# Performance work log

Hardware: AMD Instinct MI355X
Metric: run time of the kernel (lower is better)

The kernel has to match this reference:

```python
import jax, jax.numpy as jnp
import numpy as np

FEATURE_DIM = 1024
N_HEADS = 16
D_K = 64
D_V = 64
B = 8
S = 1024
LN_EPS = 1e-5
NEG = 1e9


def setup_inputs() -> dict:
    key = jax.random.key(0)
    ks = jax.random.split(key, 7)
    sc = 0.02
    return {
        "input_Q": jax.random.normal(ks[0], (B, S, FEATURE_DIM), jnp.float32),
        "input_K": jax.random.normal(ks[1], (B, S, FEATURE_DIM), jnp.float32),
        "input_V": jax.random.normal(ks[2], (B, S, FEATURE_DIM), jnp.float32),
        "attn_mask": jnp.ones((B, S, S), jnp.float32),
        "W_Q": jax.random.normal(ks[3], (FEATURE_DIM, N_HEADS * D_K), jnp.float32) * sc,
        "W_K": jax.random.normal(ks[4], (FEATURE_DIM, N_HEADS * D_K), jnp.float32) * sc,
        "W_V": jax.random.normal(ks[5], (FEATURE_DIM, N_HEADS * D_V), jnp.float32) * sc,
        "W_O": jax.random.normal(ks[6], (N_HEADS * D_V, FEATURE_DIM), jnp.float32) * sc,
    }


def reference(input_Q, input_K, input_V, attn_mask, W_Q, W_K, W_V, W_O):
    b = input_Q.shape[0]
    # projections -> [b, h, s, d]
    Q = (input_Q @ W_Q).reshape(b, -1, N_HEADS, D_K).transpose(0, 2, 1, 3)
    K = (input_K @ W_K).reshape(b, -1, N_HEADS, D_K).transpose(0, 2, 1, 3)
    V = (input_V @ W_V).reshape(b, -1, N_HEADS, D_V).transpose(0, 2, 1, 3)
    # scores [b, h, sq, sk]
    scores = jnp.einsum("bhqd,bhkd->bhqk", Q, K) / np.sqrt(D_K).astype(np.float32)
    # additive mask: (mask - 1) * 1e9, broadcast over heads
    scores = scores + (attn_mask[:, None, :, :] - 1.0) * NEG
    attn = jax.nn.softmax(scores, axis=-1)
    # dropout is eval-mode identity (deterministic baseline)
    context = jnp.einsum("bhqk,bhkd->bhqd", attn, V)
    context = context.transpose(0, 2, 1, 3).reshape(b, -1, N_HEADS * D_V)
    output = context @ W_O
    x = output + input_Q  # residual
    # fresh nn.LayerNorm(feature_dim): weight=1, bias=0
    mu = jnp.mean(x, axis=-1, keepdims=True)
    var = jnp.var(x, axis=-1, keepdims=True)
    out = (x - mu) * jax.lax.rsqrt(var + LN_EPS)
    return out, attn
```

## Files before the change

### kernel.cpp

```cpp
#include <hip/hip_runtime.h>
#include <hip/hip_bf16.h>
#include <stdint.h>

typedef unsigned short u16;
typedef unsigned int u32;
typedef __attribute__((ext_vector_type(8))) short bf16x8;
typedef __attribute__((ext_vector_type(4))) float f32x4;

#define BATCH 8
#define SEQ   1024
#define FDIM  1024
#define NHEAD 16
#define DHEAD 64

__device__ __forceinline__ float bf2f(u16 u) {
  union { unsigned int i; float f; } v; v.i = ((unsigned int)u) << 16; return v.f;
}
__device__ __forceinline__ u16 f2bf(float f) {
  union { float f; unsigned int i; } v; v.f = f;
  unsigned int x = v.i;
  return (u16)((x + 0x7fffu + ((x >> 16) & 1u)) >> 16);
}

__device__ __forceinline__ uint4 load8(const u16* p) { return *(const uint4*)p; }
__device__ __forceinline__ uint4 load8(const float* p) {
  float4 a = *(const float4*)p;
  float4 b = *(const float4*)(p + 4);
  union { u16 h[8]; uint4 v; } r;
  r.h[0] = f2bf(a.x); r.h[1] = f2bf(a.y); r.h[2] = f2bf(a.z); r.h[3] = f2bf(a.w);
  r.h[4] = f2bf(b.x); r.h[5] = f2bf(b.y); r.h[6] = f2bf(b.z); r.h[7] = f2bf(b.w);
  return r.v;
}

__device__ __forceinline__ void gload16(const u16* g, u16* l) {
  __builtin_amdgcn_global_load_lds(
      (__attribute__((address_space(1))) u32*)(u16*)g,
      (__attribute__((address_space(3))) u32*)l, 16, 0, 0);
}

__global__ __launch_bounds__(256) void cvt_k(
    const float* __restrict__ in, u16* __restrict__ out) {
  const long i = ((long)blockIdx.x * 256 + threadIdx.x) * 8;
  *(uint4*)&out[i] = load8(&in[i]);
}

__global__ __launch_bounds__(256) void transpose_k(
    const float* __restrict__ src, u16* __restrict__ dst, int srcLd, int dstLd) {
  __shared__ u16 t[64][72];
  const int r0 = blockIdx.y * 64, c0 = blockIdx.x * 64;
  const int tid = threadIdx.x;
  for (int p = 0; p < 16; ++p) {
    int idx = p * 256 + tid, r = idx >> 6, c = idx & 63;
    t[r][c] = f2bf(src[(long)(r0 + r) * srcLd + (c0 + c)]);
  }
  __syncthreads();
  for (int p = 0; p < 16; ++p) {
    int idx = p * 256 + tid, r = idx >> 6, c = idx & 63;
    dst[(long)(c0 + r) * dstLd + (r0 + c)] = t[c][r];
  }
}

template<int MODE>
__global__ __launch_bounds__(256) void gemm16(
    const u16* __restrict__ A, const u16* __restrict__ Bt, void* __restrict__ C,
    int K, int lda, int ldb, int ldc) {
  __shared__ __align__(16) u16 As[128 * 32];
  __shared__ __align__(16) u16 Bs[128 * 32];
  const int tid = threadIdx.x;
  const int wave = tid >> 6, lane = tid & 63;
  const int quad = lane >> 4, l16 = lane & 15;
  const int wm = wave >> 1, wn = wave & 1;
  const int bid = blockIdx.y * 8 + blockIdx.x;
  const int cpx = (gridDim.y * 8) >> 3;
  const int swz = (bid & 7) * cpx + (bid >> 3);
  const int m0 = (swz >> 3) * 128, n0 = (swz & 7) * 128;

  f32x4 acc[4][4];
#pragma unroll
  for (int i = 0; i < 4; ++i)
#pragma unroll
    for (int j = 0; j < 4; ++j) acc[i][j] = (f32x4){0.f, 0.f, 0.f, 0.f};

  const int srow = lane >> 2, scol = (lane & 3) * 8;
  const u16* ga = &A[(long)(m0 + wave * 32 + srow) * lda + scol];
  const u16* gb = &Bt[(long)(n0 + wave * 32 + srow) * ldb + scol];
  u16* la0 = &As[(wave * 32) * 32];
  u16* la1 = &As[(wave * 32 + 16) * 32];
  u16* lb0 = &Bs[(wave * 32) * 32];
  u16* lb1 = &Bs[(wave * 32 + 16) * 32];

  for (int k0 = 0; k0 < K; k0 += 32) {
    __syncthreads();
    gload16(ga + k0,            la0);
    gload16(ga + k0 + 16 * lda, la1);
    gload16(gb + k0,            lb0);
    gload16(gb + k0 + 16 * ldb, lb1);
    __syncthreads();
    bf16x8 af[4], bfr[4];
#pragma unroll
    for (int i = 0; i < 4; ++i)
      af[i] = *(const bf16x8*)&As[(wm * 64 + i * 16 + l16) * 32 + quad * 8];
#pragma unroll
    for (int j = 0; j < 4; ++j)
      bfr[j] = *(const bf16x8*)&Bs[(wn * 64 + j * 16 + l16) * 32 + quad * 8];
#pragma unroll
    for (int i = 0; i < 4; ++i)
#pragma unroll
      for (int j = 0; j < 4; ++j)
        acc[i][j] = __builtin_amdgcn_mfma_f32_16x16x32_bf16(af[i], bfr[j], acc[i][j], 0, 0, 0);
  }

#pragma unroll
  for (int i = 0; i < 4; ++i) {
    const int rowb = m0 + wm * 64 + i * 16 + quad * 4;
#pragma unroll
    for (int j = 0; j < 4; ++j) {
      const int col = n0 + wn * 64 + j * 16 + l16;
#pragma unroll
      for (int r = 0; r < 4; ++r) {
        const float v = acc[i][j][r];
        const int row = rowb + r;
        if (MODE == 1) {
          ((float*)C)[(long)row * ldc + col] = v;
        } else if (MODE == 2) {
          int bb = row >> 10, ss = row & 1023, hh = col >> 6, dd = col & 63;
          ((u16*)C)[((long)(bb * NHEAD + hh) * SEQ + ss) * DHEAD + dd] = f2bf(v);
        } else if (MODE == 3) {
          int bb = row >> 10, ss = row & 1023, hh = col >> 6, dd = col & 63;
          ((u16*)C)[((long)(bb * NHEAD + hh) * DHEAD + dd) * SEQ + ss] = f2bf(v);
        } else {
          ((u16*)C)[(long)row * ldc + col] = f2bf(v);
        }
      }
    }
  }
}

__global__ __launch_bounds__(256, 4) void attn_kernel(
    const u16* __restrict__ Qb, const u16* __restrict__ Kb,
    const u16* __restrict__ Vt, const float* __restrict__ Msk,
    float* __restrict__ P, u16* __restrict__ Ctx) {
  __shared__ __align__(16) u16 QVs[64][72];
  __shared__ __align__(16) u16 Ks[64][72];
  __shared__ __align__(16) float Ps[64][68];
  const int tid = threadIdx.x, wave = tid >> 6, lane = tid & 63;
  const int quad = lane >> 4, l16 = lane & 15;
  const int q0 = blockIdx.x * 64, h = blockIdx.y, b = blockIdx.z;
  const long bh = (long)b * NHEAD + h;
  const u16* Qp = Qb + ((long)b * SEQ + q0) * FDIM + h * DHEAD;
  const u16* Kp = Kb + bh * SEQ * DHEAD;
  const u16* Vp = Vt + bh * (long)DHEAD * SEQ;
  const float* Mp = Msk + ((long)b * SEQ + q0) * SEQ;
  float* Pp = P + bh * (long)SEQ * SEQ + (long)q0 * SEQ;
  u16* Cp = Ctx + ((long)b * SEQ + q0) * FDIM + h * DHEAD;

  {
    int r = tid >> 3, c = (tid & 7) * 8;
    *(uint4*)&QVs[r][c]      = *(const uint4*)&Qp[(long)r * FDIM + c];
    *(uint4*)&QVs[r + 32][c] = *(const uint4*)&Qp[(long)(r + 32) * FDIM + c];
  }
  __syncthreads();
  const bf16x8 aq0 = *(const bf16x8*)&QVs[wave * 16 + l16][quad * 8];
  const bf16x8 aq1 = *(const bf16x8*)&QVs[wave * 16 + l16][32 + quad * 8];

  float m[4], l[4], rl[4];
#pragma unroll
  for (int r = 0; r < 4; ++r) { m[r] = -3.0e38f; l[r] = 0.f; }

  for (int st = 0; st < SEQ / 64; ++st) {
    const int sk0 = st * 64;
    __syncthreads();
    {
      int r = tid >> 3, c = (tid & 7) * 8;
      *(uint4*)&Ks[r][c]      = *(const uint4*)&Kp[(sk0 + r) * DHEAD + c];
      *(uint4*)&Ks[r + 32][c] = *(const uint4*)&Kp[(sk0 + r + 32) * DHEAD + c];
    }
    __syncthreads();
    float sv[4][4];
#pragma unroll
    for (int j = 0; j < 4; ++j) {
      bf16x8 bk0 = *(const bf16x8*)&Ks[j * 16 + l16][quad * 8];
      bf16x8 bk1 = *(const bf16x8*)&Ks[j * 16 + l16][32 + quad * 8];
      f32x4 sc = (f32x4){0.f, 0.f, 0.f, 0.f};
      sc = __builtin_amdgcn_mfma_f32_16x16x32_bf16(aq0, bk0, sc, 0, 0, 0);
      sc = __builtin_amdgcn_mfma_f32_16x16x32_bf16(aq1, bk1, sc, 0, 0, 0);
#pragma unroll
      for (int r = 0; r < 4; ++r) {
        int qr = wave * 16 + quad * 4 + r;
        float mk = Mp[(long)qr * SEQ + sk0 + j * 16 + l16];
        sv[j][r] = sc[r] * 0.125f + (mk - 1.0f) * 1.0e9f;
      }
    }
#pragma unroll
    for (int r = 0; r < 4; ++r) {
      float tm = fmaxf(fmaxf(sv[0][r], sv[1][r]), fmaxf(sv[2][r], sv[3][r]));
#pragma unroll
      for (int off = 1; off < 16; off <<= 1) tm = fmaxf(tm, __shfl_xor(tm, off, 64));
      float mn = fmaxf(m[r], tm);
      float ps = __expf(sv[0][r] - mn) + __expf(sv[1][r] - mn) +
                 __expf(sv[2][r] - mn) + __expf(sv[3][r] - mn);
#pragma unroll
      for (int off = 1; off < 16; off <<= 1) ps += __shfl_xor(ps, off, 64);
      l[r] = l[r] * __expf(m[r] - mn) + ps;
      m[r] = mn;
    }
  }
#pragma unroll
  for (int r = 0; r < 4; ++r) rl[r] = 1.0f / l[r];

  f32x4 acc[4];
#pragma unroll
  for (int n = 0; n < 4; ++n) acc[n] = (f32x4){0.f, 0.f, 0.f, 0.f};

  for (int st = 0; st < SEQ / 64; ++st) {
    const int sk0 = st * 64;
    __syncthreads();
    {
      int r = tid >> 3, c = (tid & 7) * 8;
      *(uint4*)&Ks[r][c]       = *(const uint4*)&Kp[(sk0 + r) * DHEAD + c];
      *(uint4*)&Ks[r + 32][c]  = *(const uint4*)&Kp[(sk0 + r + 32) * DHEAD + c];
      *(uint4*)&QVs[r][c]      = *(const uint4*)&Vp[(long)r * SEQ + sk0 + c];
      *(uint4*)&QVs[r + 32][c] = *(const uint4*)&Vp[(long)(r + 32) * SEQ + sk0 + c];
    }
    __syncthreads();
#pragma unroll
    for (int j = 0; j < 4; ++j) {
      bf16x8 bk0 = *(const bf16x8*)&Ks[j * 16 + l16][quad * 8];
      bf16x8 bk1 = *(const bf16x8*)&Ks[j * 16 + l16][32 + quad * 8];
      f32x4 sc = (f32x4){0.f, 0.f, 0.f, 0.f};
      sc = __builtin_amdgcn_mfma_f32_16x16x32_bf16(aq0, bk0, sc, 0, 0, 0);
      sc = __builtin_amdgcn_mfma_f32_16x16x32_bf16(aq1, bk1, sc, 0, 0, 0);
#pragma unroll
      for (int r = 0; r < 4; ++r) {
        int qr = wave * 16 + quad * 4 + r;
        float mk = Mp[(long)qr * SEQ + sk0 + j * 16 + l16];
        float s = sc[r] * 0.125f + (mk - 1.0f) * 1.0e9f;
        Ps[qr][j * 16 + l16] = __expf(s - m[r]) * rl[r];
      }
    }
    __syncthreads();
#pragma unroll
    for (int ks = 0; ks < 2; ++ks) {
      const float* pr = &Ps[wave * 16 + l16][ks * 32 + quad * 8];
      f32x4 plo = *(const f32x4*)pr;
      f32x4 phi = *(const f32x4*)(pr + 4);
      union { u16 h[8]; bf16x8 v; } pa;
      pa.h[0] = f2bf(plo.x); pa.h[1] = f2bf(plo.y);
      pa.h[2] = f2bf(plo.z); pa.h[3] = f2bf(plo.w);
      pa.h[4] = f2bf(phi.x); pa.h[5] = f2bf(phi.y);
      pa.h[6] = f2bf(phi.z); pa.h[7] = f2bf(phi.w);
#pragma unroll
      for (int n = 0; n < 4; ++n) {
        bf16x8 bv = *(const bf16x8*)&QVs[n * 16 + l16][ks * 32 + quad * 8];
        acc[n] = __builtin_amdgcn_mfma_f32_16x16x32_bf16(pa.v, bv, acc[n], 0, 0, 0);
      }
    }
#pragma unroll
    for (int rr = 0; rr < 4; ++rr) {
      const int row = wave * 16 + rr * 4 + quad;
      f32x4 val = *(const f32x4*)&Ps[row][l16 * 4];
      __builtin_nontemporal_store(val, (f32x4*)&Pp[(long)row * SEQ + sk0 + l16 * 4]);
    }
  }

#pragma unroll
  for (int n = 0; n < 4; ++n)
#pragma unroll
    for (int r = 0; r < 4; ++r)
      Cp[(long)(wave * 16 + quad * 4 + r) * FDIM + n * 16 + l16] = f2bf(acc[n][r]);
}

__global__ __launch_bounds__(256) void ln_kernel(
    const float* __restrict__ O, const float* __restrict__ Xq, float* __restrict__ out) {
  const int row = blockIdx.x, tid = threadIdx.x;
  const float4 o = *(const float4*)&O[(long)row * FDIM + tid * 4];
  const float4 q = *(const float4*)&Xq[(long)row * FDIM + tid * 4];
  float x[4] = { o.x + q.x, o.y + q.y, o.z + q.z, o.w + q.w };
  float s  = x[0] + x[1] + x[2] + x[3];
  float s2 = x[0]*x[0] + x[1]*x[1] + x[2]*x[2] + x[3]*x[3];
#pragma unroll
  for (int off = 32; off; off >>= 1) {
    s  += __shfl_xor(s, off, 64);
    s2 += __shfl_xor(s2, off, 64);
  }
  __shared__ float red[8];
  const int wave = tid >> 6, lane = tid & 63;
  if (lane == 0) { red[wave] = s; red[4 + wave] = s2; }
  __syncthreads();
  s  = red[0] + red[1] + red[2] + red[3];
  s2 = red[4] + red[5] + red[6] + red[7];
  const float mu = s * (1.0f / FDIM);
  const float var = s2 * (1.0f / FDIM) - mu * mu;
  const float rs = rsqrtf(var + 1e-5f);
  float4 res;
  res.x = (x[0] - mu) * rs; res.y = (x[1] - mu) * rs;
  res.z = (x[2] - mu) * rs; res.w = (x[3] - mu) * rs;
  *(float4*)&out[(long)row * FDIM + tid * 4] = res;
}

extern "C" void kernel_launch(void* const* d_in, const int* in_sizes, int n_in,
                              void* d_out, int out_size, void* d_ws, size_t ws_size,
                              hipStream_t stream) {
  const float* Xq = (const float*)d_in[0];
  const float* Xk = (const float*)d_in[1];
  const float* Xv = (const float*)d_in[2];
  const float* Mk = (const float*)d_in[3];
  const float* Wq = (const float*)d_in[4];
  const float* Wk = (const float*)d_in[5];
  const float* Wv = (const float*)d_in[6];
  const float* Wo = (const float*)d_in[7];

  u16* ws  = (u16*)d_ws;
  const size_t M = 1u << 20;
  u16* WtQ = ws;
  u16* WtK = ws + 1 * M;
  u16* WtV = ws + 2 * M;
  u16* WtO = ws + 3 * M;
  u16* Qb  = ws + 4 * M;
  u16* Kb  = ws + 12 * M;
  u16* Vt  = ws + 20 * M;
  float* O = (float*)(ws + 12 * M);

  float* out = (float*)d_out;
  float* P   = out + (size_t)BATCH * SEQ * FDIM;

  u16* Xqb = (u16*)P;
  u16* Xkb = (u16*)P + 8 * M;
  u16* Xvb = (u16*)P + 16 * M;

  cvt_k<<<dim3(4096, 1, 1), 256, 0, stream>>>(Xq, Xqb);
  cvt_k<<<dim3(4096, 1, 1), 256, 0, stream>>>(Xk, Xkb);
  cvt_k<<<dim3(4096, 1, 1), 256, 0, stream>>>(Xv, Xvb);
  transpose_k<<<dim3(16, 16, 1), 256, 0, stream>>>(Wq, WtQ, FDIM, FDIM);
  transpose_k<<<dim3(16, 16, 1), 256, 0, stream>>>(Wk, WtK, FDIM, FDIM);
  transpose_k<<<dim3(16, 16, 1), 256, 0, stream>>>(Wv, WtV, FDIM, FDIM);
  transpose_k<<<dim3(16, 16, 1), 256, 0, stream>>>(Wo, WtO, FDIM, FDIM);
  gemm16<4><<<dim3(8, 64, 1), 256, 0, stream>>>(Xqb, WtQ, Qb, FDIM, FDIM, FDIM, FDIM);
  gemm16<2><<<dim3(8, 64, 1), 256, 0, stream>>>(Xkb, WtK, Kb, FDIM, FDIM, FDIM, 0);
  gemm16<3><<<dim3(8, 64, 1), 256, 0, stream>>>(Xvb, WtV, Vt, FDIM, FDIM, FDIM, 0);
  attn_kernel<<<dim3(SEQ / 64, NHEAD, BATCH), 256, 0, stream>>>(Qb, Kb, Vt, Mk, P, Qb);
  gemm16<1><<<dim3(8, 64, 1), 256, 0, stream>>>(Qb, WtO, O, FDIM, FDIM, FDIM, FDIM);
  ln_kernel<<<dim3(BATCH * SEQ, 1, 1), 256, 0, stream>>>(O, Xq, out);
}
```

Before: 1.004 ms.

## Prefetch next K/V/mask tiles into registers and drop redundant barrier

Both passes of the attention kernel now load the next iteration's K, V and mask tiles into registers while computing on the current tile, instead of loading and then stalling on a barrier. The aim is to hide global-memory latency behind the MFMA and softmax work. The barrier between writing and reading the probability tile is removed, which is safe because each wave only touches its own rows. MFMA sections are also wrapped in s_setprio. The cost is more registers, which may lower occupancy, plus one redundant wrap-around load per pass.

New measurement: 926.7 us. 7.7% less time.

```diff
diff --git a/kernel.cpp b/kernel.cpp
--- a/kernel.cpp
+++ b/kernel.cpp
@@ -154,10 +154,12 @@
   float* Pp = P + bh * (long)SEQ * SEQ + (long)q0 * SEQ;
   u16* Cp = Ctx + ((long)b * SEQ + q0) * FDIM + h * DHEAD;
 
+  const int lr = tid >> 3, lc = (tid & 7) * 8;
+  const int qrb = wave * 16 + quad * 4;
+
   {
-    int r = tid >> 3, c = (tid & 7) * 8;
-    *(uint4*)&QVs[r][c]      = *(const uint4*)&Qp[(long)r * FDIM + c];
-    *(uint4*)&QVs[r + 32][c] = *(const uint4*)&Qp[(long)(r + 32) * FDIM + c];
+    *(uint4*)&QVs[lr][lc]      = *(const uint4*)&Qp[(long)lr * FDIM + lc];
+    *(uint4*)&QVs[lr + 32][lc] = *(const uint4*)&Qp[(long)(lr + 32) * FDIM + lc];
   }
   __syncthreads();
   const bf16x8 aq0 = *(const bf16x8*)&QVs[wave * 16 + l16][quad * 8];
@@ -167,29 +169,43 @@
 #pragma unroll
   for (int r = 0; r < 4; ++r) { m[r] = -3.0e38f; l[r] = 0.f; }
 
+  uint4 kr0 = *(const uint4*)&Kp[lr * DHEAD + lc];
+  uint4 kr1 = *(const uint4*)&Kp[(lr + 32) * DHEAD + lc];
+  float mc[4][4];
+#pragma unroll
+  for (int j = 0; j < 4; ++j)
+#pragma unroll
+    for (int r = 0; r < 4; ++r)
+      mc[j][r] = Mp[(long)(qrb + r) * SEQ + j * 16 + l16];
+
   for (int st = 0; st < SEQ / 64; ++st) {
-    const int sk0 = st * 64;
-    __syncthreads();
-    {
-      int r = tid >> 3, c = (tid & 7) * 8;
-      *(uint4*)&Ks[r][c]      = *(const uint4*)&Kp[(sk0 + r) * DHEAD + c];
-      *(uint4*)&Ks[r + 32][c] = *(const uint4*)&Kp[(sk0 + r + 32) * DHEAD + c];
-    }
-    __syncthreads();
+    __syncthreads();
+    *(uint4*)&Ks[lr][lc]      = kr0;
+    *(uint4*)&Ks[lr + 32][lc] = kr1;
+    __syncthreads();
+    const int skn = ((st + 1) & 15) * 64;
+    kr0 = *(const uint4*)&Kp[(skn + lr) * DHEAD + lc];
+    kr1 = *(const uint4*)&Kp[(skn + lr + 32) * DHEAD + lc];
+    float mn_[4][4];
+#pragma unroll
+    for (int j = 0; j < 4; ++j)
+#pragma unroll
+      for (int r = 0; r < 4; ++r)
+        mn_[j][r] = Mp[(long)(qrb + r) * SEQ + skn + j * 16 + l16];
+
     float sv[4][4];
 #pragma unroll
     for (int j = 0; j < 4; ++j) {
       bf16x8 bk0 = *(const bf16x8*)&Ks[j * 16 + l16][quad * 8];
       bf16x8 bk1 = *(const bf16x8*)&Ks[j * 16 + l16][32 + quad * 8];
       f32x4 sc = (f32x4){0.f, 0.f, 0.f, 0.f};
+      __builtin_amdgcn_s_setprio(1);
       sc = __builtin_amdgcn_mfma_f32_16x16x32_bf16(aq0, bk0, sc, 0, 0, 0);
       sc = __builtin_amdgcn_mfma_f32_16x16x32_bf16(aq1, bk1, sc, 0, 0, 0);
-#pragma unroll
-      for (int r = 0; r < 4; ++r) {
-        int qr = wave * 16 + quad * 4 + r;
-        float mk = Mp[(long)qr * SEQ + sk0 + j * 16 + l16];
-        sv[j][r] = sc[r] * 0.125f + (mk - 1.0f) * 1.0e9f;
-      }
+      __builtin_amdgcn_s_setprio(0);
+#pragma unroll
+      for (int r = 0; r < 4; ++r)
+        sv[j][r] = sc[r] * 0.125f + (mc[j][r] - 1.0f) * 1.0e9f;
     }
 #pragma unroll
     for (int r = 0; r < 4; ++r) {
@@ -204,7 +220,21 @@
       l[r] = l[r] * __expf(m[r] - mn) + ps;
       m[r] = mn;
     }
-  }
+#pragma unroll
+    for (int j = 0; j < 4; ++j)
+#pragma unroll
+      for (int r = 0; r < 4; ++r) mc[j][r] = mn_[j][r];
+  }
+
+  kr0 = *(const uint4*)&Kp[lr * DHEAD + lc];
+  kr1 = *(const uint4*)&Kp[(lr + 32) * DHEAD + lc];
+  uint4 vr0 = *(const uint4*)&Vp[(long)lr * SEQ + lc];
+  uint4 vr1 = *(const uint4*)&Vp[(long)(lr + 32) * SEQ + lc];
+#pragma unroll
+  for (int j = 0; j < 4; ++j)
+#pragma unroll
+    for (int r = 0; r < 4; ++r)
+      mc[j][r] = Mp[(long)(qrb + r) * SEQ + j * 16 + l16];
 #pragma unroll
   for (int r = 0; r < 4; ++r) rl[r] = 1.0f / l[r];
 
@@ -215,30 +245,38 @@
   for (int st = 0; st < SEQ / 64; ++st) {
     const int sk0 = st * 64;
     __syncthreads();
-    {
-      int r = tid >> 3, c = (tid & 7) * 8;
-      *(uint4*)&Ks[r][c]       = *(const uint4*)&Kp[(sk0 + r) * DHEAD + c];
-      *(uint4*)&Ks[r + 32][c]  = *(const uint4*)&Kp[(sk0 + r + 32) * DHEAD + c];
-      *(uint4*)&QVs[r][c]      = *(const uint4*)&Vp[(long)r * SEQ + sk0 + c];
-      *(uint4*)&QVs[r + 32][c] = *(const uint4*)&Vp[(long)(r + 32) * SEQ + sk0 + c];
-    }
-    __syncthreads();
+    *(uint4*)&Ks[lr][lc]       = kr0;
+    *(uint4*)&Ks[lr + 32][lc]  = kr1;
+    *(uint4*)&QVs[lr][lc]      = vr0;
+    *(uint4*)&QVs[lr + 32][lc] = vr1;
+    __syncthreads();
+    const int skn = ((st + 1) & 15) * 64;
+    kr0 = *(const uint4*)&Kp[(skn + lr) * DHEAD + lc];
+    kr1 = *(const uint4*)&Kp[(skn + lr + 32) * DHEAD + lc];
+    vr0 = *(const uint4*)&Vp[(long)lr * SEQ + skn + lc];
+    vr1 = *(const uint4*)&Vp[(long)(lr + 32) * SEQ + skn + lc];
+    float mn_[4][4];
+#pragma unroll
+    for (int j = 0; j < 4; ++j)
+#pragma unroll
+      for (int r = 0; r < 4; ++r)
+        mn_[j][r] = Mp[(long)(qrb + r) * SEQ + skn + j * 16 + l16];
+
 #pragma unroll
     for (int j = 0; j < 4; ++j) {
       bf16x8 bk0 = *(const bf16x8*)&Ks[j * 16 + l16][quad * 8];
       bf16x8 bk1 = *(const bf16x8*)&Ks[j * 16 + l16][32 + quad * 8];
       f32x4 sc = (f32x4){0.f, 0.f, 0.f, 0.f};
+      __builtin_amdgcn_s_setprio(1);
       sc = __builtin_amdgcn_mfma_f32_16x16x32_bf16(aq0, bk0, sc, 0, 0, 0);
       sc = __builtin_amdgcn_mfma_f32_16x16x32_bf16(aq1, bk1, sc, 0, 0, 0);
+      __builtin_amdgcn_s_setprio(0);
 #pragma unroll
       for (int r = 0; r < 4; ++r) {
-        int qr = wave * 16 + quad * 4 + r;
-        float mk = Mp[(long)qr * SEQ + sk0 + j * 16 + l16];
-        float s = sc[r] * 0.125f + (mk - 1.0f) * 1.0e9f;
-        Ps[qr][j * 16 + l16] = __expf(s - m[r]) * rl[r];
+        float s = sc[r] * 0.125f + (mc[j][r] - 1.0f) * 1.0e9f;
+        Ps[qrb + r][j * 16 + l16] = __expf(s - m[r]) * rl[r];
       }
     }
-    __syncthreads();
 #pragma unroll
     for (int ks = 0; ks < 2; ++ks) {
       const float* pr = &Ps[wave * 16 + l16][ks * 32 + quad * 8];
@@ -249,11 +287,13 @@
       pa.h[2] = f2bf(plo.z); pa.h[3] = f2bf(plo.w);
       pa.h[4] = f2bf(phi.x); pa.h[5] = f2bf(phi.y);
       pa.h[6] = f2bf(phi.z); pa.h[7] = f2bf(phi.w);
+      __builtin_amdgcn_s_setprio(1);
 #pragma unroll
       for (int n = 0; n < 4; ++n) {
         bf16x8 bv = *(const bf16x8*)&QVs[n * 16 + l16][ks * 32 + quad * 8];
         acc[n] = __builtin_amdgcn_mfma_f32_16x16x32_bf16(pa.v, bv, acc[n], 0, 0, 0);
       }
+      __builtin_amdgcn_s_setprio(0);
     }
 #pragma unroll
     for (int rr = 0; rr < 4; ++rr) {
@@ -261,13 +301,17 @@
       f32x4 val = *(const f32x4*)&Ps[row][l16 * 4];
       __builtin_nontemporal_store(val, (f32x4*)&Pp[(long)row * SEQ + sk0 + l16 * 4]);
     }
+#pragma unroll
+    for (int j = 0; j < 4; ++j)
+#pragma unroll
+      for (int r = 0; r < 4; ++r) mc[j][r] = mn_[j][r];
   }
 
 #pragma unroll
   for (int n = 0; n < 4; ++n)
 #pragma unroll
     for (int r = 0; r < 4; ++r)
-      Cp[(long)(wave * 16 + quad * 4 + r) * FDIM + n * 16 + l16] = f2bf(acc[n][r]);
+      Cp[(long)(qrb + r) * FDIM + n * 16 + l16] = f2bf(acc[n][r]);
 }
 
 __global__ __launch_bounds__(256) void ln_kernel(
```
